# Kernel optimization log

Measured on AMD Instinct MI355X. Metric: run time of the kernel, lower is better.

Reference implementation:

```python
import jax, jax.numpy as jnp
import numpy as np

B, S, HID = 1, 2048, 4096
H, KV, D, R = 32, 8, 128, 64   # heads, kv heads, head_dim, rotary_dim
EPS = 1e-6
THETA = 10000.0


def setup_inputs() -> dict:
    key = jax.random.key(0)
    ks = jax.random.split(key, 6)
    sc = 0.02
    return {
        'hidden_states': jax.random.normal(ks[0], (B, S, HID), jnp.float32),
        'Wq': jax.random.normal(ks[1], (H * D, HID), jnp.float32) * sc,
        'Wk': jax.random.normal(ks[2], (KV * D, HID), jnp.float32) * sc,
        'Wv': jax.random.normal(ks[3], (KV * D, HID), jnp.float32) * sc,
        'Wo': jax.random.normal(ks[4], (HID, H * D), jnp.float32) * sc,
        'q_norm_w': jnp.ones((H * D,), jnp.float32),
        'k_norm_w': jnp.ones((KV * D,), jnp.float32),
        'position_ids': jnp.broadcast_to(jnp.arange(S, dtype=jnp.int64)[None, :], (B, S)),
    }


def _rms_norm(x, w):
    xf = x.astype(jnp.float32)
    var = jnp.mean(xf * xf, axis=-1, keepdims=True)
    return (w * (xf * jax.lax.rsqrt(var + EPS))).astype(x.dtype)


def _rotate_half(x):
    x1, x2 = x[..., : R // 2], x[..., R // 2:]
    return jnp.concatenate((-x2, x1), axis=-1)


def reference(hidden_states, Wq, Wk, Wv, Wo, q_norm_w, k_norm_w, position_ids):
    x = hidden_states
    # projections (torch Linear: y = x @ W^T)
    q = jnp.einsum('bsd,od->bso', x, Wq)                      # [B,S,H*D]
    k = jnp.einsum('bsd,od->bso', x, Wk)                      # [B,S,KV*D]
    v = jnp.einsum('bsd,od->bso', x, Wv).reshape(B, S, KV, D)
    # QK RMSNorm over flattened head dims
    q = _rms_norm(q, q_norm_w).reshape(B, S, H, D)
    k = _rms_norm(k, k_norm_w).reshape(B, S, KV, D)
    # partial RoPE: rotary_dim=R out of head_dim=D
    inv_freq = 1.0 / (THETA ** (jnp.arange(0, R, 2, dtype=jnp.float32) / R))  # [R/2]
    freqs = position_ids.astype(jnp.float32)[..., None] * inv_freq            # [B,S,R/2]
    emb = jnp.concatenate((freqs, freqs), axis=-1)                            # [B,S,R]
    cos = jnp.cos(emb)[:, :, None, :]                                         # [B,S,1,R]
    sin = jnp.sin(emb)[:, :, None, :]
    q_rot = q[..., :R] * cos + _rotate_half(q[..., :R]) * sin
    k_rot = k[..., :R] * cos + _rotate_half(k[..., :R]) * sin
    q = jnp.concatenate((q_rot, q[..., R:]), axis=-1)
    k = jnp.concatenate((k_rot, k[..., R:]), axis=-1)
    # GQA repeat_kv
    G = H // KV
    k = jnp.repeat(k, G, axis=2)  # [B,S,H,D]
    v = jnp.repeat(v, G, axis=2)
    # attention with causal mask, softmax in fp32
    scaling = D ** -0.5
    scores = jnp.einsum('bqhd,bkhd->bhqk', q, k) * scaling    # [B,H,S,S]
    causal = jnp.tril(jnp.ones((S, S), dtype=bool))
    scores = jnp.where(causal[None, None], scores, jnp.finfo(jnp.float32).min)
    attn = jax.nn.softmax(scores.astype(jnp.float32), axis=-1).astype(q.dtype)
    out = jnp.einsum('bhqk,bkhd->bqhd', attn, v).reshape(B, S, H * D)
    return jnp.einsum('bso,do->bsd', out, Wo)
```

## Files before the change

kernel.cpp:

```cpp
#include <hip/hip_runtime.h>
#include <hip/hip_bf16.h>
#include <math.h>

typedef __bf16 bf16;
typedef __bf16 bf16x8 __attribute__((ext_vector_type(8)));
typedef float f32x4 __attribute__((ext_vector_type(4)));
typedef float f32x16 __attribute__((ext_vector_type(16)));

#define S_LEN 2048
#define HID_D 4096
#define NH 32
#define NKV 8
#define HD 128
#define SCALE_LOG2 (0.08838834764831843f * 1.4426950408889634f)
#define FIXED_M 17.0f

__device__ __forceinline__ void gload_lds16(const void* g, void* lds) {
  __builtin_amdgcn_global_load_lds((__attribute__((address_space(1))) void*)g,
                                   (__attribute__((address_space(3))) void*)lds, 16, 0, 0);
}

#define MEMFENCE asm volatile("" ::: "memory")

__global__ __launch_bounds__(256) void cvt_kernel(const float* __restrict__ in,
                                                  bf16* __restrict__ out, int n8) {
  int i = blockIdx.x * blockDim.x + threadIdx.x;
  int stride = gridDim.x * blockDim.x;
  for (; i < n8; i += stride) {
    const float4* p = (const float4*)in + 2 * (size_t)i;
    float4 a = p[0], b = p[1];
    bf16x8 o;
    o[0] = (bf16)a.x; o[1] = (bf16)a.y; o[2] = (bf16)a.z; o[3] = (bf16)a.w;
    o[4] = (bf16)b.x; o[5] = (bf16)b.y; o[6] = (bf16)b.z; o[7] = (bf16)b.w;
    *((bf16x8*)out + i) = o;
  }
}

template <int BM, int BN>
__global__ __launch_bounds__(512, 2) void gemm_s(const bf16* __restrict__ A,
                                                 const bf16* __restrict__ B,
                                                 float* __restrict__ C,
                                                 int N, int Kfull, int T) {
  constexpr int MFr = BM / 32;
  constexpr int NFr = BN / 64;
  constexpr int NL = (BM + BN) / 64;
  constexpr int TILE = (BM + BN) * 128;

  __shared__ __align__(16) char lds[2 * TILE];
  const int t = threadIdx.x, l = t & 63, w = t >> 6;
  const int wr = w >> 2, wc = w & 3;
  const int l15 = l & 15, lg = l >> 4;

  const int GX = gridDim.x, GY = gridDim.y;
  const int lin = blockIdx.y * GX + blockIdx.x;
  const int x = lin & 7, j = lin >> 3;
  const int rectW = GX >> 2, rectH = GY >> 1;
  const int rx = x & 3, ry = x >> 2;
  const int jn = j % rectW, jm = j / rectW;
  const int n0 = (rx * rectW + jn) * BN;
  const int m0 = (ry * rectH + jm) * BM;

  auto stage = [&](int d, int tau) {
    char* dst = lds + d * TILE;
    const size_t kpos = (size_t)tau * 64;
#pragma unroll
    for (int i = 0; i < NL; i++) {
      int q = i * 512 + t;
      int r = q >> 3;
      int c = (q & 7) ^ (r & 7);
      const bf16* src = (i * 512 < BM * 8)
                            ? (A + (size_t)(m0 + r) * Kfull)
                            : (B + (size_t)(n0 + (r - BM)) * Kfull);
      gload_lds16(src + kpos + c * 8, dst + q * 16);
    }
  };

  f32x4 acc[MFr][NFr] = {};

  stage(0, 0);
  asm volatile("s_waitcnt vmcnt(0)" ::: "memory");
  MEMFENCE; __builtin_amdgcn_s_barrier(); MEMFENCE;

  for (int tau = 0; tau < T; tau++) {
    const int d = tau & 1;
    if (tau + 1 < T) stage(d ^ 1, tau + 1);

    const char* Ab = lds + d * TILE;
    const char* Bb = Ab + BM * 128;
    bf16x8 a[MFr][2], b[NFr][2];
#pragma unroll
    for (int mf = 0; mf < MFr; mf++) {
      const int row = wr * (BM / 2) + mf * 16 + l15;
#pragma unroll
      for (int ks = 0; ks < 2; ks++)
        a[mf][ks] = *(const bf16x8*)(Ab + row * 128 + (((ks * 4 + lg) ^ (row & 7)) << 4));
    }
#pragma unroll
    for (int nf = 0; nf < NFr; nf++) {
      const int row = wc * (BN / 4) + nf * 16 + l15;
#pragma unroll
      for (int ks = 0; ks < 2; ks++)
        b[nf][ks] = *(const bf16x8*)(Bb + row * 128 + (((ks * 4 + lg) ^ (row & 7)) << 4));
    }
#pragma unroll
    for (int mf = 0; mf < MFr; mf++)
#pragma unroll
      for (int nf = 0; nf < NFr; nf++)
#pragma unroll
        for (int ks = 0; ks < 2; ks++)
          acc[mf][nf] = __builtin_amdgcn_mfma_f32_16x16x32_bf16(a[mf][ks], b[nf][ks],
                                                               acc[mf][nf], 0, 0, 0);

    asm volatile("s_waitcnt vmcnt(0)" ::: "memory");
    MEMFENCE; __builtin_amdgcn_s_barrier(); MEMFENCE;
  }

#pragma unroll
  for (int mf = 0; mf < MFr; mf++) {
    int row = m0 + wr * (BM / 2) + mf * 16 + lg * 4;
#pragma unroll
    for (int nf = 0; nf < NFr; nf++) {
      int col = n0 + wc * (BN / 4) + nf * 16 + l15;
      float* Cp = C + (size_t)row * N + col;
#pragma unroll
      for (int rr = 0; rr < 4; rr++) Cp[(size_t)rr * N] = acc[mf][nf][rr];
    }
  }
}

__global__ __launch_bounds__(256) void vt_kernel(const float* __restrict__ QKV,
                                                 bf16* __restrict__ Vt) {
  __shared__ __align__(16) float tile[64][68];
  const int s0 = blockIdx.x * 64, d0 = blockIdx.y * 64;
  const int t = threadIdx.x;
#pragma unroll
  for (int i = 0; i < 4; i++) {
    int row = i * 16 + (t >> 4);
    int c4 = t & 15;
    float4 v = *(const float4*)(QKV + (size_t)(s0 + row) * 6144 + 5120 + d0 + c4 * 4);
    *(float4*)&tile[row][c4 * 4] = v;
  }
  __syncthreads();
#pragma unroll
  for (int i = 0; i < 2; i++) {
    int slot = i * 256 + t;
    int dr = slot >> 3, ch = slot & 7;
    bf16x8 o;
#pragma unroll
    for (int j = 0; j < 8; j++) o[j] = (bf16)tile[ch * 8 + j][dr];
    *(bf16x8*)(Vt + (size_t)(d0 + dr) * S_LEN + s0 + ch * 8) = o;
  }
}

__global__ __launch_bounds__(256) void prep_kernel(const float* __restrict__ QKV,
                                                   const float* __restrict__ qw,
                                                   const float* __restrict__ kw,
                                                   const int* __restrict__ pos_ids,
                                                   bf16* __restrict__ Qb,
                                                   bf16* __restrict__ Kb) {
  __shared__ __align__(16) float row[5120];
  __shared__ float cs[64];
  __shared__ float red[8];
  const int s = blockIdx.x, t = threadIdx.x;

  const float4* src = (const float4*)(QKV + (size_t)s * 6144);
#pragma unroll
  for (int i = 0; i < 5; i++) ((float4*)row)[t + i * 256] = src[t + i * 256];

  if (t < 32) {
    float p = (float)pos_ids[s];
    float ang = p * powf(10000.0f, -(float)t * (1.0f / 32.0f));
    float sn, cn;
    sincosf(ang, &sn, &cn);
    cs[t] = cn;
    cs[32 + t] = sn;
  }
  __syncthreads();

  float aq = 0.f, ak = 0.f;
  for (int i = t; i < 4096; i += 256) { float v = row[i]; aq += v * v; }
  for (int i = 4096 + t; i < 5120; i += 256) { float v = row[i]; ak += v * v; }
#pragma unroll
  for (int off = 32; off; off >>= 1) {
    aq += __shfl_down(aq, off);
    ak += __shfl_down(ak, off);
  }
  if ((t & 63) == 0) { red[t >> 6] = aq; red[4 + (t >> 6)] = ak; }
  __syncthreads();
  const float scq = rsqrtf((red[0] + red[1] + red[2] + red[3]) * (1.0f / 4096.0f) + 1e-6f);
  const float sck = rsqrtf((red[4] + red[5] + red[6] + red[7]) * (1.0f / 1024.0f) + 1e-6f);

  for (int e = t; e < 4096; e += 256) {
    int d = e & 127;
    int hh = e >> 7;
    float val = row[e] * scq * qw[e];
    float o;
    if (d < 32)       o = val * cs[d] - (row[e + 32] * scq * qw[e + 32]) * cs[32 + d];
    else if (d < 64)  o = val * cs[d - 32] + (row[e - 32] * scq * qw[e - 32]) * cs[d];
    else              o = val;
    Qb[((size_t)hh * S_LEN + s) * HD + d] = (bf16)o;
  }
  for (int e = t; e < 1024; e += 256) {
    int d = e & 127;
    int hh = e >> 7;
    int ri = 4096 + e;
    float val = row[ri] * sck * kw[e];
    float o;
    if (d < 32)       o = val * cs[d] - (row[ri + 32] * sck * kw[e + 32]) * cs[32 + d];
    else if (d < 64)  o = val * cs[d - 32] + (row[ri - 32] * sck * kw[e - 32]) * cs[d];
    else              o = val;
    Kb[((size_t)hh * S_LEN + s) * HD + d] = (bf16)o;
  }
}

__global__ __launch_bounds__(256, 2) void attn_kernel(const bf16* __restrict__ Qb,
                                                      const bf16* __restrict__ Kb,
                                                      const bf16* __restrict__ Vt,
                                                      bf16* __restrict__ Ctx) {
  __shared__ __align__(16) char KB[2][16384];
  __shared__ __align__(16) char VB[16384];
  __shared__ __align__(16) char PB[16384];
  const int t = threadIdx.x, l = t & 63, w = t >> 6;
  const int l31 = l & 31, hi = l >> 5;
  const int pairc = blockIdx.x >> 5;
  const int h = blockIdx.x & 31;

  const bf16* Kh = Kb + (size_t)(h >> 2) * S_LEN * HD;
  const bf16* Vh = Vt + (size_t)(h >> 2) * HD * S_LEN;
  char* Pw = PB + w * 4096;

  const int kj0 = t & 15;
  const int vj0 = t & 7;

  auto stageK = [&](int buf, int kvbase) {
#pragma unroll
    for (int i = 0; i < 4; i++) {
      int r = (i * 256 + t) >> 4;
      const bf16* src = Kh + (size_t)(kvbase + r) * HD + ((kj0 ^ (r & 7)) << 3);
      gload_lds16(src, KB[buf] + (i * 256 + w * 64) * 16);
    }
  };
  auto stageV = [&](int kvbase) {
#pragma unroll
    for (int i = 0; i < 4; i++) {
      int r = (i * 256 + t) >> 3;
      const bf16* src = Vh + (size_t)r * S_LEN + kvbase + ((vj0 ^ (r & 7)) << 3);
      gload_lds16(src, VB + (i * 256 + w * 64) * 16);
    }
  };

#pragma unroll
  for (int phase = 0; phase < 2; phase++) {
    const int chunk = (phase == 0) ? pairc : (15 - pairc);
    const int ktiles = 2 * chunk + 2;
    const int q0 = chunk * 128 + w * 32;

    const bf16* Qh = Qb + ((size_t)h * S_LEN + q0) * HD;
    bf16x8 qf[8];
#pragma unroll
    for (int j = 0; j < 8; j++)
      qf[j] = *(const bf16x8*)(Qh + (size_t)l31 * HD + j * 16 + hi * 8);

    stageK(0, 0);

    f32x16 O[4] = {};
    float lsum[16] = {};

    for (int tt = 0; tt < ktiles; tt++) {
      const int cur = tt & 1;
      const int kv0 = tt * 64;
      const char* Kcur = KB[cur];
      const bool hasnext = (tt + 1 < ktiles);

      MEMFENCE;
      __builtin_amdgcn_s_barrier();
      MEMFENCE;

      stageV(kv0);
      if (hasnext) {
        stageK(cur ^ 1, kv0 + 64);
        asm volatile("s_waitcnt vmcnt(8)" ::: "memory");
      } else {
        asm volatile("s_waitcnt vmcnt(4)" ::: "memory");
      }
      MEMFENCE;
      __builtin_amdgcn_s_barrier();
      MEMFENCE;

      f32x16 sc[2] = {};
      __builtin_amdgcn_s_setprio(1);
#pragma unroll
      for (int n = 0; n < 2; n++) {
        const int kr = n * 32 + l31;
        const char* Krow = Kcur + kr * 256;
        const int sw = l31 & 7;
#pragma unroll
        for (int j = 0; j < 8; j++) {
          bf16x8 kf = *(const bf16x8*)(Krow + (((2 * j + hi) ^ sw) << 4));
          sc[n] = __builtin_amdgcn_mfma_f32_32x32x16_bf16(qf[j], kf, sc[n], 0, 0, 0);
        }
      }
      __builtin_amdgcn_s_setprio(0);

      const bool needmask = (kv0 + 63 > q0);
#pragma unroll
      for (int n = 0; n < 2; n++) {
        const int kv = kv0 + n * 32 + l31;
#pragma unroll
        for (int e = 0; e < 16; e++) {
          const int row = (e & 3) + 8 * (e >> 2) + 4 * hi;
          float x = fmaf(sc[n][e], SCALE_LOG2, -FIXED_M);
          if (needmask && kv > q0 + row) x = -1e30f;
          float sv = exp2f(x);
          lsum[e] += sv;
          const int chunkc = 4 * n + (l31 >> 3);
          *(bf16*)(Pw + row * 128 + (((chunkc ^ (row & 7))) << 4) + ((l31 & 7) << 1)) =
              (bf16)sv;
        }
      }
      asm volatile("s_waitcnt lgkmcnt(0)" ::: "memory");

      bf16x8 pa[4];
#pragma unroll
      for (int j = 0; j < 4; j++)
        pa[j] = *(const bf16x8*)(Pw + l31 * 128 + (((2 * j + hi) ^ (l31 & 7)) << 4));

      if (hasnext) asm volatile("s_waitcnt vmcnt(4)" ::: "memory");
      else         asm volatile("s_waitcnt vmcnt(0)" ::: "memory");
      MEMFENCE;
      __builtin_amdgcn_s_barrier();
      MEMFENCE;

      __builtin_amdgcn_s_setprio(1);
#pragma unroll
      for (int dt = 0; dt < 4; dt++) {
        const int vr = dt * 32 + l31;
        const char* Vrow = VB + vr * 128;
        const int sw = l31 & 7;
#pragma unroll
        for (int j = 0; j < 4; j++) {
          bf16x8 vf = *(const bf16x8*)(Vrow + (((2 * j + hi) ^ sw) << 4));
          O[dt] = __builtin_amdgcn_mfma_f32_32x32x16_bf16(pa[j], vf, O[dt], 0, 0, 0);
        }
      }
      __builtin_amdgcn_s_setprio(0);
    }

    MEMFENCE;
    __builtin_amdgcn_s_barrier();
    MEMFENCE;

    float inv[16];
#pragma unroll
    for (int e = 0; e < 16; e++) {
      float x = lsum[e];
      x += __shfl_xor(x, 1);
      x += __shfl_xor(x, 2);
      x += __shfl_xor(x, 4);
      x += __shfl_xor(x, 8);
      x += __shfl_xor(x, 16);
      inv[e] = 1.0f / x;
    }
#pragma unroll
    for (int dt = 0; dt < 4; dt++)
#pragma unroll
      for (int e = 0; e < 16; e++) {
        const int row = (e & 3) + 8 * (e >> 2) + 4 * hi;
        Ctx[(size_t)(q0 + row) * HID_D + h * HD + dt * 32 + l31] = (bf16)(O[dt][e] * inv[e]);
      }
  }
}

extern "C" void kernel_launch(void* const* d_in, const int* in_sizes, int n_in,
                              void* d_out, int out_size, void* d_ws, size_t ws_size,
                              hipStream_t stream) {
  const float* X  = (const float*)d_in[0];
  const float* Wq = (const float*)d_in[1];
  const float* Wk = (const float*)d_in[2];
  const float* Wv = (const float*)d_in[3];
  const float* Wo = (const float*)d_in[4];
  const float* qw = (const float*)d_in[5];
  const float* kw = (const float*)d_in[6];
  const int* pos  = (const int*)d_in[7];

  char* ws = (char*)d_ws;
  bf16* Xb    = (bf16*)ws;
  bf16* Wqkvb = (bf16*)(ws + (16ll << 20));
  bf16* Wob   = Wqkvb;
  float* QKV  = (float*)(ws + (64ll << 20));
  bf16* Ctx   = (bf16*)(ws + (96ll << 20));
  bf16* Qb    = (bf16*)(ws + (112ll << 20));
  bf16* Kb    = (bf16*)(ws + (128ll << 20));
  bf16* Vt    = (bf16*)(ws + (132ll << 20));

  cvt_kernel<<<2048, 256, 0, stream>>>(X, Xb, S_LEN * HID_D / 8);
  cvt_kernel<<<2048, 256, 0, stream>>>(Wq, Wqkvb, 4096 * 4096 / 8);
  cvt_kernel<<<512, 256, 0, stream>>>(Wk, Wqkvb + 4096 * 4096, 1024 * 4096 / 8);
  cvt_kernel<<<512, 256, 0, stream>>>(Wv, Wqkvb + 5120 * 4096, 1024 * 4096 / 8);

  gemm_s<128, 384><<<dim3(16, 16), 512, 0, stream>>>(Xb, Wqkvb, QKV, 6144, HID_D, 64);

  cvt_kernel<<<2048, 256, 0, stream>>>(Wo, Wob, 4096 * 4096 / 8);

  vt_kernel<<<dim3(32, 16), 256, 0, stream>>>(QKV, Vt);
  prep_kernel<<<S_LEN, 256, 0, stream>>>(QKV, qw, kw, pos, Qb, Kb);

  attn_kernel<<<dim3(256), 256, 0, stream>>>(Qb, Kb, Vt, Ctx);

  gemm_s<128, 256><<<dim3(16, 16), 512, 0, stream>>>(Ctx, Wob, (float*)d_out,
                                                     HID_D, HID_D, 64);
}
```

Measured before the change: 359.7 us.

## Split attention KV range across two blocks and combine partial outputs

Attention blocks now process only even or odd 64-wide KV tiles (selected by z), doubling the grid from 256 to 512 blocks. Each split writes unnormalized bf16 context and per-row sums, and a new combine kernel adds the two partials and normalizes. The LDS swizzle also gains an extra XOR bit, apparently to reduce bank conflicts. This adds a combine pass and extra global traffic (two bf16 context buffers plus sums), and rounds partial outputs to bf16 before they are summed.

```diff
diff --git a/kernel.cpp b/kernel.cpp
--- a/kernel.cpp
+++ b/kernel.cpp
@@ -36,6 +36,28 @@
   }
 }
 
+__global__ __launch_bounds__(256) void combine_kernel(const bf16* __restrict__ C0,
+                                                      const bf16* __restrict__ C1,
+                                                      const float* __restrict__ L0,
+                                                      const float* __restrict__ L1,
+                                                      bf16* __restrict__ Ctx) {
+  int i = blockIdx.x * blockDim.x + threadIdx.x;
+  int stride = gridDim.x * blockDim.x;
+  const int n8 = S_LEN * HID_D / 8;
+  for (; i < n8; i += stride) {
+    int q = (i * 8) >> 12;
+    int col = (i * 8) & (HID_D - 1);
+    int h = col >> 7;
+    float inv = 1.0f / (L0[(size_t)h * S_LEN + q] + L1[(size_t)h * S_LEN + q]);
+    bf16x8 a = ((const bf16x8*)C0)[i];
+    bf16x8 b = ((const bf16x8*)C1)[i];
+    bf16x8 o;
+#pragma unroll
+    for (int j = 0; j < 8; j++) o[j] = (bf16)(((float)a[j] + (float)b[j]) * inv);
+    ((bf16x8*)Ctx)[i] = o;
+  }
+}
+
 template <int BM, int BN>
 __global__ __launch_bounds__(512, 2) void gemm_s(const bf16* __restrict__ A,
                                                  const bf16* __restrict__ B,
@@ -216,43 +238,50 @@
 __global__ __launch_bounds__(256, 2) void attn_kernel(const bf16* __restrict__ Qb,
                                                       const bf16* __restrict__ Kb,
                                                       const bf16* __restrict__ Vt,
-                                                      bf16* __restrict__ Ctx) {
+                                                      bf16* __restrict__ CtxZ,
+                                                      float* __restrict__ LsumZ) {
   __shared__ __align__(16) char KB[2][16384];
   __shared__ __align__(16) char VB[16384];
   __shared__ __align__(16) char PB[16384];
   const int t = threadIdx.x, l = t & 63, w = t >> 6;
   const int l31 = l & 31, hi = l >> 5;
-  const int pairc = blockIdx.x >> 5;
+  const int z = blockIdx.x >> 8;
+  const int pairc = (blockIdx.x >> 5) & 7;
   const int h = blockIdx.x & 31;
 
   const bf16* Kh = Kb + (size_t)(h >> 2) * S_LEN * HD;
   const bf16* Vh = Vt + (size_t)(h >> 2) * HD * S_LEN;
+  bf16* Ctx = CtxZ + (size_t)z * S_LEN * HID_D;
+  float* Lsum = LsumZ + (size_t)z * NH * S_LEN;
   char* Pw = PB + w * 4096;
 
   const int kj0 = t & 15;
   const int vj0 = t & 7;
+  const int swl = (l31 & 7) ^ (((l31 >> 3) & 1) << 2);
 
   auto stageK = [&](int buf, int kvbase) {
 #pragma unroll
     for (int i = 0; i < 4; i++) {
       int r = (i * 256 + t) >> 4;
-      const bf16* src = Kh + (size_t)(kvbase + r) * HD + ((kj0 ^ (r & 7)) << 3);
-      gload_lds16(src, KB[buf] + (i * 256 + w * 64) * 16);
+      int c = kj0 ^ (r & 7) ^ (((r >> 3) & 1) << 2);
+      gload_lds16(Kh + (size_t)(kvbase + r) * HD + (c << 3),
+                  KB[buf] + (i * 256 + w * 64) * 16);
     }
   };
   auto stageV = [&](int kvbase) {
 #pragma unroll
     for (int i = 0; i < 4; i++) {
       int r = (i * 256 + t) >> 3;
-      const bf16* src = Vh + (size_t)r * S_LEN + kvbase + ((vj0 ^ (r & 7)) << 3);
-      gload_lds16(src, VB + (i * 256 + w * 64) * 16);
+      int c = vj0 ^ (r & 7) ^ (((r >> 3) & 1) << 2);
+      gload_lds16(Vh + (size_t)r * S_LEN + kvbase + (c << 3),
+                  VB + (i * 256 + w * 64) * 16);
     }
   };
 
 #pragma unroll
   for (int phase = 0; phase < 2; phase++) {
     const int chunk = (phase == 0) ? pairc : (15 - pairc);
-    const int ktiles = 2 * chunk + 2;
+    const int cnt = chunk + 1;
     const int q0 = chunk * 128 + w * 32;
 
     const bf16* Qh = Qb + ((size_t)h * S_LEN + q0) * HD;
@@ -261,16 +290,16 @@
     for (int j = 0; j < 8; j++)
       qf[j] = *(const bf16x8*)(Qh + (size_t)l31 * HD + j * 16 + hi * 8);
 
-    stageK(0, 0);
+    stageK(0, z * 64);
 
     f32x16 O[4] = {};
     float lsum[16] = {};
 
-    for (int tt = 0; tt < ktiles; tt++) {
-      const int cur = tt & 1;
-      const int kv0 = tt * 64;
+    for (int i = 0; i < cnt; i++) {
+      const int cur = i & 1;
+      const int kv0 = (2 * i + z) * 64;
       const char* Kcur = KB[cur];
-      const bool hasnext = (tt + 1 < ktiles);
+      const bool hasnext = (i + 1 < cnt);
 
       MEMFENCE;
       __builtin_amdgcn_s_barrier();
@@ -278,7 +307,7 @@
 
       stageV(kv0);
       if (hasnext) {
-        stageK(cur ^ 1, kv0 + 64);
+        stageK(cur ^ 1, kv0 + 128);
         asm volatile("s_waitcnt vmcnt(8)" ::: "memory");
       } else {
         asm volatile("s_waitcnt vmcnt(4)" ::: "memory");
@@ -291,12 +320,10 @@
       __builtin_amdgcn_s_setprio(1);
 #pragma unroll
       for (int n = 0; n < 2; n++) {
-        const int kr = n * 32 + l31;
-        const char* Krow = Kcur + kr * 256;
-        const int sw = l31 & 7;
+        const char* Krow = Kcur + (n * 32 + l31) * 256;
 #pragma unroll
         for (int j = 0; j < 8; j++) {
-          bf16x8 kf = *(const bf16x8*)(Krow + (((2 * j + hi) ^ sw) << 4));
+          bf16x8 kf = *(const bf16x8*)(Krow + (((2 * j + hi) ^ swl) << 4));
           sc[n] = __builtin_amdgcn_mfma_f32_32x32x16_bf16(qf[j], kf, sc[n], 0, 0, 0);
         }
       }
@@ -313,9 +340,8 @@
           if (needmask && kv > q0 + row) x = -1e30f;
           float sv = exp2f(x);
           lsum[e] += sv;
-          const int chunkc = 4 * n + (l31 >> 3);
-          *(bf16*)(Pw + row * 128 + (((chunkc ^ (row & 7))) << 4) + ((l31 & 7) << 1)) =
-              (bf16)sv;
+          const int slot = (4 * n + (l31 >> 3)) ^ (row & 7) ^ (((row >> 3) & 1) << 2);
+          *(bf16*)(Pw + row * 128 + (slot << 4) + ((l31 & 7) << 1)) = (bf16)sv;
         }
       }
       asm volatile("s_waitcnt lgkmcnt(0)" ::: "memory");
@@ -323,7 +349,7 @@
       bf16x8 pa[4];
 #pragma unroll
       for (int j = 0; j < 4; j++)
-        pa[j] = *(const bf16x8*)(Pw + l31 * 128 + (((2 * j + hi) ^ (l31 & 7)) << 4));
+        pa[j] = *(const bf16x8*)(Pw + l31 * 128 + (((2 * j + hi) ^ swl) << 4));
 
       if (hasnext) asm volatile("s_waitcnt vmcnt(4)" ::: "memory");
       else         asm volatile("s_waitcnt vmcnt(0)" ::: "memory");
@@ -334,12 +360,10 @@
       __builtin_amdgcn_s_setprio(1);
 #pragma unroll
       for (int dt = 0; dt < 4; dt++) {
-        const int vr = dt * 32 + l31;
-        const char* Vrow = VB + vr * 128;
-        const int sw = l31 & 7;
+        const char* Vrow = VB + (dt * 32 + l31) * 128;
 #pragma unroll
         for (int j = 0; j < 4; j++) {
-          bf16x8 vf = *(const bf16x8*)(Vrow + (((2 * j + hi) ^ sw) << 4));
+          bf16x8 vf = *(const bf16x8*)(Vrow + (((2 * j + hi) ^ swl) << 4));
           O[dt] = __builtin_amdgcn_mfma_f32_32x32x16_bf16(pa[j], vf, O[dt], 0, 0, 0);
         }
       }
@@ -350,7 +374,7 @@
     __builtin_amdgcn_s_barrier();
     MEMFENCE;
 
-    float inv[16];
+    float red[16];
 #pragma unroll
     for (int e = 0; e < 16; e++) {
       float x = lsum[e];
@@ -359,14 +383,21 @@
       x += __shfl_xor(x, 4);
       x += __shfl_xor(x, 8);
       x += __shfl_xor(x, 16);
-      inv[e] = 1.0f / x;
-    }
-#pragma unroll
-    for (int dt = 0; dt < 4; dt++)
+      red[e] = x;
+    }
+    if (l31 == 0) {
 #pragma unroll
       for (int e = 0; e < 16; e++) {
         const int row = (e & 3) + 8 * (e >> 2) + 4 * hi;
-        Ctx[(size_t)(q0 + row) * HID_D + h * HD + dt * 32 + l31] = (bf16)(O[dt][e] * inv[e]);
+        Lsum[(size_t)h * S_LEN + q0 + row] = red[e];
+      }
+    }
+#pragma unroll
+    for (int dt = 0; dt < 4; dt++)
+#pragma unroll
+      for (int e = 0; e < 16; e++) {
+        const int row = (e & 3) + 8 * (e >> 2) + 4 * hi;
+        Ctx[(size_t)(q0 + row) * HID_D + h * HD + dt * 32 + l31] = (bf16)O[dt][e];
       }
   }
 }
@@ -387,7 +418,10 @@
   bf16* Xb    = (bf16*)ws;
   bf16* Wqkvb = (bf16*)(ws + (16ll << 20));
   bf16* Wob   = Wqkvb;
+  float* Ls0  = (float*)(ws + (48ll << 20));
+  float* Ls1  = Ls0 + (size_t)NH * S_LEN;
   float* QKV  = (float*)(ws + (64ll << 20));
+  bf16* Ctx01 = (bf16*)(ws + (64ll << 20));
   bf16* Ctx   = (bf16*)(ws + (96ll << 20));
   bf16* Qb    = (bf16*)(ws + (112ll << 20));
   bf16* Kb    = (bf16*)(ws + (128ll << 20));
@@ -405,7 +439,9 @@
   vt_kernel<<<dim3(32, 16), 256, 0, stream>>>(QKV, Vt);
   prep_kernel<<<S_LEN, 256, 0, stream>>>(QKV, qw, kw, pos, Qb, Kb);
 
-  attn_kernel<<<dim3(256), 256, 0, stream>>>(Qb, Kb, Vt, Ctx);
+  attn_kernel<<<dim3(512), 256, 0, stream>>>(Qb, Kb, Vt, Ctx01, Ls0);
+  combine_kernel<<<2048, 256, 0, stream>>>(Ctx01, Ctx01 + (size_t)S_LEN * HID_D,
+                                           Ls0, Ls1, Ctx);
 
   gemm_s<128, 256><<<dim3(16, 16), 512, 0, stream>>>(Ctx, Wob, (float*)d_out,
                                                      HID_D, HID_D, 64);
```

New measurement: 344.0 us. 1.05x faster.
